# Kernel optimization log

Hardware: AMD Instinct MI355X
Metric: run time of the kernel (lower is better)

The kernel has to match this reference:

```python
import jax, jax.numpy as jnp
import numpy as np

N = 100000   # nodes
E = 1000000  # edges
F = 128      # num_features
H = 64       # hidden_size
C = 1        # num_classes
G = 128      # num graphs in batch


def gcn_conv(x, W, b, src, dst, deg_inv_sqrt):
    # PyG GCNConv: add self-loops, symmetric normalization D^-1/2 (A+I) D^-1/2, then X W + b
    h = x @ W                                   # [N, H]
    norm = deg_inv_sqrt[src] * deg_inv_sqrt[dst]  # [E]
    msg = h[src] * norm[:, None]                # gather + scale, [E, H]
    out = jnp.zeros_like(h).at[dst].add(msg)    # scatter-add to targets
    out = out + h * (deg_inv_sqrt ** 2)[:, None]  # self-loop contribution
    return out + b


def setup_inputs() -> dict:
    key = jax.random.key(0)
    ks = jax.random.split(key, 12)
    x = jax.random.normal(ks[0], (N, F), dtype=jnp.float32)
    edge_index = jax.random.randint(ks[1], (2, E), 0, N, dtype=jnp.int32).astype(jnp.int64)
    batch = jnp.sort(jax.random.randint(ks[2], (N,), 0, G, dtype=jnp.int32)).astype(jnp.int64)
    def glorot(k, fan_in, fan_out):
        s = np.float32(np.sqrt(6.0 / (fan_in + fan_out)))
        return jax.random.uniform(k, (fan_in, fan_out), jnp.float32, -s, s)
    return {
        "x": x, "edge_index": edge_index, "batch": batch,
        "W1": glorot(ks[3], F, H), "b1": jnp.zeros((H,), jnp.float32),
        "W2": glorot(ks[4], H, H), "b2": jnp.zeros((H,), jnp.float32),
        "Wl1": glorot(ks[5], H, H), "bl1": jnp.zeros((H,), jnp.float32),
        "Wl2": glorot(ks[6], H, C), "bl2": jnp.zeros((C,), jnp.float32),
    }


def reference(x, edge_index, batch, W1, b1, W2, b2, Wl1, bl1, Wl2, bl2):
    src, dst = edge_index[0], edge_index[1]
    # degree with self-loops: 1 + in-degree(target)
    deg = jnp.ones((N,), x.dtype).at[dst].add(jnp.ones((E,), x.dtype))
    deg_inv_sqrt = jax.lax.rsqrt(deg)
    h = jax.nn.relu(gcn_conv(x, W1, b1, src, dst, deg_inv_sqrt))
    h = jax.nn.relu(gcn_conv(h, W2, b2, src, dst, deg_inv_sqrt))
    g = jax.ops.segment_sum(h, batch, num_segments=G)  # global_add_pool, [G, H]
    g = jax.nn.relu(g @ Wl1 + bl1)
    out = g @ Wl2 + bl2                                # [G, 1]
    return out.squeeze(axis=1)                         # [G]
```

## Files before the change

### kernel.cpp

```cpp
#include <hip/hip_runtime.h>

#define NN 100000
#define EE 1000000
#define FF 128
#define HH 64
#define GG 128
#define NB 391

__device__ inline unsigned short f2bf(float f) {
    unsigned u = __float_as_uint(f);
    u += 0x7fffu + ((u >> 16) & 1u);
    return (unsigned short)(u >> 16);
}
__device__ inline float bf2f(unsigned short h) {
    return __uint_as_float((unsigned)h << 16);
}

__global__ void k_hist(const int* __restrict__ ei, int* __restrict__ cnt) {
    int e = blockIdx.x * 256 + threadIdx.x;
    if (e < EE) atomicAdd(&cnt[ei[EE + e]], 1);
}

__global__ void k_scan1(const int* __restrict__ cnt, int* __restrict__ part) {
    int i = blockIdx.x * 256 + threadIdx.x;
    int v = (i < NN) ? cnt[i] : 0;
    for (int o = 1; o < 64; o <<= 1) v += __shfl_xor(v, o);
    __shared__ int ws[4];
    if ((threadIdx.x & 63) == 0) ws[threadIdx.x >> 6] = v;
    __syncthreads();
    if (threadIdx.x == 0) part[blockIdx.x] = ws[0] + ws[1] + ws[2] + ws[3];
}

__global__ void k_scan2(int* __restrict__ part) {
    __shared__ int buf[512];
    int t = threadIdx.x;
    int v = (t < NB) ? part[t] : 0;
    buf[t] = v; __syncthreads();
    for (int o = 1; o < 512; o <<= 1) {
        int u = (t >= o) ? buf[t - o] : 0;
        __syncthreads();
        buf[t] += u;
        __syncthreads();
    }
    if (t < NB) part[t] = buf[t] - v;
}

__global__ void k_scan3(const int* __restrict__ cnt, const int* __restrict__ part,
                        int* __restrict__ row_ptr, int* __restrict__ cursor,
                        float* __restrict__ dis) {
    int i = blockIdx.x * 256 + threadIdx.x;
    int v = (i < NN) ? cnt[i] : 0;
    int lane = threadIdx.x & 63, w = threadIdx.x >> 6;
    int incl = v;
    for (int o = 1; o < 64; o <<= 1) { int u = __shfl_up(incl, o); if (lane >= o) incl += u; }
    __shared__ int ws[4];
    if (lane == 63) ws[w] = incl;
    __syncthreads();
    int woff = 0;
    for (int k = 0; k < w; ++k) woff += ws[k];
    int excl = incl - v + woff + part[blockIdx.x];
    if (i < NN) {
        row_ptr[i] = excl;
        cursor[i]  = excl;
        dis[i] = rsqrtf((float)(v + 1));
    }
    if (i == 0) row_ptr[NN] = EE;
}

__global__ void k_place(const int* __restrict__ ei, int* __restrict__ cursor,
                        int* __restrict__ srcs) {
    int e = blockIdx.x * 256 + threadIdx.x;
    if (e < EE) {
        int d = ei[EE + e];
        int p = atomicAdd(&cursor[d], 1);
        srcs[p] = ei[e];
    }
}

template<int K>
__global__ __launch_bounds__(256) void
k_matmul_b(const float* __restrict__ X, const float* __restrict__ W,
           const float* __restrict__ dis, unsigned short* __restrict__ Y) {
    __shared__ float Wl[K * HH];
    for (int i = threadIdx.x; i < K * HH; i += 256) Wl[i] = W[i];
    __syncthreads();
    const int lane = threadIdx.x & 63;
    const int wv   = threadIdx.x >> 6;
    const int c4   = (lane & 15) * 4;
    const int rsg  = lane >> 4;
    const int r0   = blockIdx.x * 64 + wv * 16 + rsg * 4;

    const float* xr0; const float* xr1; const float* xr2; const float* xr3;
    {
        int a = r0,     b_ = r0 + 1, c = r0 + 2, d = r0 + 3;
        if (a > NN - 1) a = NN - 1;
        if (b_ > NN - 1) b_ = NN - 1;
        if (c > NN - 1) c = NN - 1;
        if (d > NN - 1) d = NN - 1;
        xr0 = X + (size_t)a * K; xr1 = X + (size_t)b_ * K;
        xr2 = X + (size_t)c * K; xr3 = X + (size_t)d * K;
    }
    float4 acc0 = {0,0,0,0}, acc1 = {0,0,0,0}, acc2 = {0,0,0,0}, acc3 = {0,0,0,0};

#pragma unroll 8
    for (int k4 = 0; k4 < K / 4; ++k4) {
        const float4 x0 = *(const float4*)(xr0 + k4 * 4);
        const float4 x1 = *(const float4*)(xr1 + k4 * 4);
        const float4 x2 = *(const float4*)(xr2 + k4 * 4);
        const float4 x3 = *(const float4*)(xr3 + k4 * 4);
        const float4 w0 = *(const float4*)&Wl[(k4 * 4 + 0) * HH + c4];
        const float4 w1 = *(const float4*)&Wl[(k4 * 4 + 1) * HH + c4];
        const float4 w2 = *(const float4*)&Wl[(k4 * 4 + 2) * HH + c4];
        const float4 w3 = *(const float4*)&Wl[(k4 * 4 + 3) * HH + c4];
#define FMA4(A, XS) \
        A.x = fmaf(XS.x, w0.x, A.x); A.y = fmaf(XS.x, w0.y, A.y); \
        A.z = fmaf(XS.x, w0.z, A.z); A.w = fmaf(XS.x, w0.w, A.w); \
        A.x = fmaf(XS.y, w1.x, A.x); A.y = fmaf(XS.y, w1.y, A.y); \
        A.z = fmaf(XS.y, w1.z, A.z); A.w = fmaf(XS.y, w1.w, A.w); \
        A.x = fmaf(XS.z, w2.x, A.x); A.y = fmaf(XS.z, w2.y, A.y); \
        A.z = fmaf(XS.z, w2.z, A.z); A.w = fmaf(XS.z, w2.w, A.w); \
        A.x = fmaf(XS.w, w3.x, A.x); A.y = fmaf(XS.w, w3.y, A.y); \
        A.z = fmaf(XS.w, w3.z, A.z); A.w = fmaf(XS.w, w3.w, A.w);
        FMA4(acc0, x0) FMA4(acc1, x1) FMA4(acc2, x2) FMA4(acc3, x3)
#undef FMA4
    }
#define STORE(I, A) { \
        const int r = r0 + I; \
        if (r < NN) { \
            const float d = dis[r]; \
            ushort4 o; \
            o.x = f2bf(A.x * d); o.y = f2bf(A.y * d); \
            o.z = f2bf(A.z * d); o.w = f2bf(A.w * d); \
            *(ushort4*)(Y + (size_t)r * HH + c4) = o; \
        } }
    STORE(0, acc0) STORE(1, acc1) STORE(2, acc2) STORE(3, acc3)
#undef STORE
}

template<bool POOL>
__global__ __launch_bounds__(256) void
k_gconv(const int* __restrict__ row_ptr, const int* __restrict__ srcs,
        const float* __restrict__ dis, const unsigned short* __restrict__ Hs,
        const float* __restrict__ b, float* __restrict__ Out,
        const int* __restrict__ batch, float* __restrict__ g) {
    const int node = blockIdx.x * 4 + (threadIdx.x >> 6);
    const int lane = threadIdx.x & 63;
    const int li   = lane & 15;
    const int qr   = lane >> 4;
    const int p0   = row_ptr[node];
    const int deg  = row_ptr[node + 1] - p0;
    const int items  = deg + 1;
    const int nbatch = (items + 7) >> 3;

    float ac0 = 0.f, ac1 = 0.f, ac2 = 0.f, ac3 = 0.f;

#define IDX(bi, dA, dB) { \
        const int iA = 8 * (bi) + qr, iB = iA + 4; \
        dA = srcs[p0 + (iA < deg ? iA : 0)]; \
        dB = srcs[p0 + (iB < deg ? iB : 0)]; }
#define VAL(bi, sA, sB, vA, vB) { \
        const int iA = 8 * (bi) + qr, iB = iA + 4; \
        const int rA = (iA < deg) ? sA : node; \
        const int rB = (iB < deg) ? sB : node; \
        vA = *(const uint2*)(Hs + (size_t)rA * HH + li * 4); \
        vB = *(const uint2*)(Hs + (size_t)rB * HH + li * 4); }
#define CONSUME(bi, vA, vB) { \
        const int iA = 8 * (bi) + qr, iB = iA + 4; \
        const unsigned m0 = (iA <= deg) ? vA.x : 0u; \
        const unsigned m1 = (iA <= deg) ? vA.y : 0u; \
        const unsigned m2 = (iB <= deg) ? vB.x : 0u; \
        const unsigned m3 = (iB <= deg) ? vB.y : 0u; \
        ac0 += bf2f((unsigned short)m0);  ac1 += bf2f((unsigned short)(m0 >> 16)); \
        ac2 += bf2f((unsigned short)m1);  ac3 += bf2f((unsigned short)(m1 >> 16)); \
        ac0 += bf2f((unsigned short)m2);  ac1 += bf2f((unsigned short)(m2 >> 16)); \
        ac2 += bf2f((unsigned short)m3);  ac3 += bf2f((unsigned short)(m3 >> 16)); }

    int sA0, sA1, sB0, sB1;
    uint2 vA0, vA1;
    IDX(0, sA0, sA1);
    VAL(0, sA0, sA1, vA0, vA1);
    IDX(1, sB0, sB1);
    for (int bi = 1; bi < nbatch; ++bi) {
        uint2 vB0, vB1;
        VAL(bi, sB0, sB1, vB0, vB1);
        IDX(bi + 1, sB0, sB1);
        CONSUME(bi - 1, vA0, vA1);
        vA0 = vB0; vA1 = vB1;
    }
    CONSUME(nbatch - 1, vA0, vA1);
#undef IDX
#undef VAL
#undef CONSUME

    ac0 += __shfl_xor(ac0, 16); ac0 += __shfl_xor(ac0, 32);
    ac1 += __shfl_xor(ac1, 16); ac1 += __shfl_xor(ac1, 32);
    ac2 += __shfl_xor(ac2, 16); ac2 += __shfl_xor(ac2, 32);
    ac3 += __shfl_xor(ac3, 16); ac3 += __shfl_xor(ac3, 32);
    const float c0 = __shfl(ac0, lane >> 2);
    const float c1 = __shfl(ac1, lane >> 2);
    const float c2 = __shfl(ac2, lane >> 2);
    const float c3 = __shfl(ac3, lane >> 2);
    const int m = lane & 3;
    float acc = (m == 0) ? c0 : (m == 1) ? c1 : (m == 2) ? c2 : c3;

    const float dd = dis[node];
    float v = acc * dd + b[lane];
    v = fmaxf(v, 0.0f);
    if (POOL) {
        unsafeAtomicAdd(&g[(size_t)batch[node] * HH + lane], v);
    } else {
        Out[(size_t)node * HH + lane] = v;
    }
}

__global__ void k_head1(const float* __restrict__ g, const float* __restrict__ W,
                        const float* __restrict__ b, float* __restrict__ g2) {
    const int idx = blockIdx.x * 256 + threadIdx.x;
    const int row = idx >> 6;
    const int col = idx & 63;
    const float* gr = g + (size_t)row * HH;
    float acc = b[col];
#pragma unroll
    for (int k = 0; k < HH; ++k) acc = fmaf(gr[k], W[k * HH + col], acc);
    g2[idx] = acc > 0.0f ? acc : 0.0f;
}

__global__ void k_head2(const float* __restrict__ g2, const float* __restrict__ W,
                        const float* __restrict__ b, float* __restrict__ out) {
    const int r = threadIdx.x;
    if (r >= GG) return;
    const float* gr = g2 + (size_t)r * HH;
    float acc = 0.0f;
#pragma unroll
    for (int k = 0; k < HH; ++k) acc = fmaf(gr[k], W[k], acc);
    out[r] = acc + b[0];
}

extern "C" void kernel_launch(void* const* d_in, const int* in_sizes, int n_in,
                              void* d_out, int out_size, void* d_ws, size_t ws_size,
                              hipStream_t stream) {
    const float* x   = (const float*)d_in[0];
    const int*   ei  = (const int*)d_in[1];
    const int*   bat = (const int*)d_in[2];
    const float* W1  = (const float*)d_in[3];
    const float* b1  = (const float*)d_in[4];
    const float* W2  = (const float*)d_in[5];
    const float* b2  = (const float*)d_in[6];
    const float* Wl1 = (const float*)d_in[7];
    const float* bl1 = (const float*)d_in[8];
    const float* Wl2 = (const float*)d_in[9];
    const float* bl2 = (const float*)d_in[10];
    float* out = (float*)d_out;

    char* w = (char*)d_ws;
    float* dis     = (float*)(w);
    int*   cnt     = (int*)  (w + 400128);
    int*   row_ptr = (int*)  (w + 800256);
    int*   cursor  = (int*)  (w + 1200640);
    int*   part    = (int*)  (w + 1600768);
    int*   srcs    = (int*)  (w + 1602816);
    unsigned short* B = (unsigned short*)(w + 5602816);
    float* A       = (float*)(w + 31202816);
    float* g       = (float*)(w + 56802816);
    float* g2      = g + GG * HH;

    hipMemsetAsync(cnt, 0, (size_t)NN * sizeof(int), stream);
    k_hist <<<(EE + 255) / 256, 256, 0, stream>>>(ei, cnt);
    k_scan1<<<NB, 256, 0, stream>>>(cnt, part);
    k_scan2<<<1, 512, 0, stream>>>(part);
    k_scan3<<<NB, 256, 0, stream>>>(cnt, part, row_ptr, cursor, dis);
    k_place<<<(EE + 255) / 256, 256, 0, stream>>>(ei, cursor, srcs);

    k_matmul_b<FF><<<(NN + 63) / 64, 256, 0, stream>>>(x, W1, dis, B);
    k_gconv<false><<<NN / 4, 256, 0, stream>>>(row_ptr, srcs, dis, B, b1, A, nullptr, nullptr);

    k_matmul_b<HH><<<(NN + 63) / 64, 256, 0, stream>>>(A, W2, dis, B);
    hipMemsetAsync(g, 0, (size_t)GG * HH * sizeof(float), stream);
    k_gconv<true><<<NN / 4, 256, 0, stream>>>(row_ptr, srcs, dis, B, b2, nullptr, bat, g);

    k_head1<<<(GG * HH) / 256, 256, 0, stream>>>(g, Wl1, bl1, g2);
    k_head2<<<1, 128, 0, stream>>>(g2, Wl2, bl2, out);
}
```

Baseline: 319.6 us.

## Quantize hidden features to int8 with per-row scales and fuse edge placement into matmul

Stores the transformed node features as int8 with a per-row float scale instead of bf16, which halves the bytes gathered per edge in the graph-conv kernels. Merges the edge-placement kernel into the first matmul launch as extra blocks so the two run concurrently, and moves the degree rsqrt into the first scan kernel. The int8 quantization loses precision relative to bf16 and may push results past the tolerance. Because the MMB blocks launch before the placement blocks in one grid, the two kinds of work can overlap.

New measurement: 292.4 us. 8.5% less time.

```diff
diff --git a/kernel.cpp b/kernel.cpp
--- a/kernel.cpp
+++ b/kernel.cpp
@@ -6,24 +6,19 @@
 #define HH 64
 #define GG 128
 #define NB 391
-
-__device__ inline unsigned short f2bf(float f) {
-    unsigned u = __float_as_uint(f);
-    u += 0x7fffu + ((u >> 16) & 1u);
-    return (unsigned short)(u >> 16);
-}
-__device__ inline float bf2f(unsigned short h) {
-    return __uint_as_float((unsigned)h << 16);
-}
+#define MMB 1563
 
 __global__ void k_hist(const int* __restrict__ ei, int* __restrict__ cnt) {
     int e = blockIdx.x * 256 + threadIdx.x;
     if (e < EE) atomicAdd(&cnt[ei[EE + e]], 1);
 }
 
-__global__ void k_scan1(const int* __restrict__ cnt, int* __restrict__ part) {
+__global__ void k_scan1(const int* __restrict__ cnt, int* __restrict__ part,
+                        float* __restrict__ dis) {
     int i = blockIdx.x * 256 + threadIdx.x;
-    int v = (i < NN) ? cnt[i] : 0;
+    int c = (i < NN) ? cnt[i] : 0;
+    if (i < NN) dis[i] = rsqrtf((float)(c + 1));
+    int v = (i < NN) ? c : 0;
     for (int o = 1; o < 64; o <<= 1) v += __shfl_xor(v, o);
     __shared__ int ws[4];
     if ((threadIdx.x & 63) == 0) ws[threadIdx.x >> 6] = v;
@@ -46,8 +41,7 @@
 }
 
 __global__ void k_scan3(const int* __restrict__ cnt, const int* __restrict__ part,
-                        int* __restrict__ row_ptr, int* __restrict__ cursor,
-                        float* __restrict__ dis) {
+                        int* __restrict__ row_ptr, int* __restrict__ cursor) {
     int i = blockIdx.x * 256 + threadIdx.x;
     int v = (i < NN) ? cnt[i] : 0;
     int lane = threadIdx.x & 63, w = threadIdx.x >> 6;
@@ -62,33 +56,22 @@
     if (i < NN) {
         row_ptr[i] = excl;
         cursor[i]  = excl;
-        dis[i] = rsqrtf((float)(v + 1));
     }
     if (i == 0) row_ptr[NN] = EE;
 }
 
-__global__ void k_place(const int* __restrict__ ei, int* __restrict__ cursor,
-                        int* __restrict__ srcs) {
-    int e = blockIdx.x * 256 + threadIdx.x;
-    if (e < EE) {
-        int d = ei[EE + e];
-        int p = atomicAdd(&cursor[d], 1);
-        srcs[p] = ei[e];
-    }
-}
-
 template<int K>
-__global__ __launch_bounds__(256) void
-k_matmul_b(const float* __restrict__ X, const float* __restrict__ W,
-           const float* __restrict__ dis, unsigned short* __restrict__ Y) {
-    __shared__ float Wl[K * HH];
+__device__ __forceinline__ void
+mm_body(const float* __restrict__ X, const float* __restrict__ W,
+        const float* __restrict__ dis, unsigned* __restrict__ Y8,
+        float* __restrict__ S, float* __restrict__ Wl, int bid) {
     for (int i = threadIdx.x; i < K * HH; i += 256) Wl[i] = W[i];
     __syncthreads();
     const int lane = threadIdx.x & 63;
     const int wv   = threadIdx.x >> 6;
     const int c4   = (lane & 15) * 4;
     const int rsg  = lane >> 4;
-    const int r0   = blockIdx.x * 64 + wv * 16 + rsg * 4;
+    const int r0   = bid * 64 + wv * 16 + rsg * 4;
 
     const float* xr0; const float* xr1; const float* xr2; const float* xr3;
     {
@@ -128,21 +111,57 @@
         const int r = r0 + I; \
         if (r < NN) { \
             const float d = dis[r]; \
-            ushort4 o; \
-            o.x = f2bf(A.x * d); o.y = f2bf(A.y * d); \
-            o.z = f2bf(A.z * d); o.w = f2bf(A.w * d); \
-            *(ushort4*)(Y + (size_t)r * HH + c4) = o; \
+            const float ax = A.x * d, ay = A.y * d, az = A.z * d, aw = A.w * d; \
+            float m = fmaxf(fmaxf(fabsf(ax), fabsf(ay)), fmaxf(fabsf(az), fabsf(aw))); \
+            m = fmaxf(m, __shfl_xor(m, 1)); m = fmaxf(m, __shfl_xor(m, 2)); \
+            m = fmaxf(m, __shfl_xor(m, 4)); m = fmaxf(m, __shfl_xor(m, 8)); \
+            const float inv = 127.0f / m; \
+            int q0 = __float2int_rn(ax * inv), q1 = __float2int_rn(ay * inv); \
+            int q2 = __float2int_rn(az * inv), q3 = __float2int_rn(aw * inv); \
+            if (m == 0.0f) { q0 = q1 = q2 = q3 = 0; } \
+            const unsigned pk = (q0 & 0xff) | ((q1 & 0xff) << 8) | \
+                                ((q2 & 0xff) << 16) | ((q3 & 0xff) << 24); \
+            Y8[(size_t)r * 16 + (c4 >> 2)] = pk; \
+            if (c4 == 0) S[r] = m * (1.0f / 127.0f); \
         } }
     STORE(0, acc0) STORE(1, acc1) STORE(2, acc2) STORE(3, acc3)
 #undef STORE
 }
 
+template<int K>
+__global__ __launch_bounds__(256) void
+k_matmul_b(const float* __restrict__ X, const float* __restrict__ W,
+           const float* __restrict__ dis, unsigned* __restrict__ Y8,
+           float* __restrict__ S) {
+    __shared__ float Wl[K * HH];
+    mm_body<K>(X, W, dis, Y8, S, Wl, blockIdx.x);
+}
+
+__global__ __launch_bounds__(256) void
+k_mm1_place(const float* __restrict__ X, const float* __restrict__ W,
+            const float* __restrict__ dis, unsigned* __restrict__ Y8,
+            float* __restrict__ S, const int* __restrict__ ei,
+            int* __restrict__ cursor, int* __restrict__ srcs) {
+    __shared__ float Wl[FF * HH];
+    if (blockIdx.x < MMB) {
+        mm_body<FF>(X, W, dis, Y8, S, Wl, blockIdx.x);
+    } else {
+        int e = (blockIdx.x - MMB) * 256 + threadIdx.x;
+        if (e < EE) {
+            int d = ei[EE + e];
+            int p = atomicAdd(&cursor[d], 1);
+            srcs[p] = ei[e];
+        }
+    }
+}
+
 template<bool POOL>
 __global__ __launch_bounds__(256) void
 k_gconv(const int* __restrict__ row_ptr, const int* __restrict__ srcs,
-        const float* __restrict__ dis, const unsigned short* __restrict__ Hs,
-        const float* __restrict__ b, float* __restrict__ Out,
-        const int* __restrict__ batch, float* __restrict__ g) {
+        const float* __restrict__ dis, const unsigned* __restrict__ H8,
+        const float* __restrict__ S, const float* __restrict__ b,
+        float* __restrict__ Out, const int* __restrict__ batch,
+        float* __restrict__ g) {
     const int node = blockIdx.x * 4 + (threadIdx.x >> 6);
     const int lane = threadIdx.x & 63;
     const int li   = lane & 15;
@@ -158,36 +177,40 @@
         const int iA = 8 * (bi) + qr, iB = iA + 4; \
         dA = srcs[p0 + (iA < deg ? iA : 0)]; \
         dB = srcs[p0 + (iB < deg ? iB : 0)]; }
-#define VAL(bi, sA, sB, vA, vB) { \
+#define VAL(bi, sA, sB, vA, vB, gA, gB) { \
         const int iA = 8 * (bi) + qr, iB = iA + 4; \
         const int rA = (iA < deg) ? sA : node; \
         const int rB = (iB < deg) ? sB : node; \
-        vA = *(const uint2*)(Hs + (size_t)rA * HH + li * 4); \
-        vB = *(const uint2*)(Hs + (size_t)rB * HH + li * 4); }
-#define CONSUME(bi, vA, vB) { \
+        vA = H8[(size_t)rA * 16 + li];  gA = S[rA]; \
+        vB = H8[(size_t)rB * 16 + li];  gB = S[rB]; }
+#define CONSUME(bi, vA, vB, gA, gB) { \
         const int iA = 8 * (bi) + qr, iB = iA + 4; \
-        const unsigned m0 = (iA <= deg) ? vA.x : 0u; \
-        const unsigned m1 = (iA <= deg) ? vA.y : 0u; \
-        const unsigned m2 = (iB <= deg) ? vB.x : 0u; \
-        const unsigned m3 = (iB <= deg) ? vB.y : 0u; \
-        ac0 += bf2f((unsigned short)m0);  ac1 += bf2f((unsigned short)(m0 >> 16)); \
-        ac2 += bf2f((unsigned short)m1);  ac3 += bf2f((unsigned short)(m1 >> 16)); \
-        ac0 += bf2f((unsigned short)m2);  ac1 += bf2f((unsigned short)(m2 >> 16)); \
-        ac2 += bf2f((unsigned short)m3);  ac3 += bf2f((unsigned short)(m3 >> 16)); }
+        const float s0 = (iA <= deg) ? gA : 0.f; \
+        const float s1 = (iB <= deg) ? gB : 0.f; \
+        ac0 = fmaf(s0, (float)(signed char)(vA      ), ac0); \
+        ac1 = fmaf(s0, (float)(signed char)(vA >> 8 ), ac1); \
+        ac2 = fmaf(s0, (float)(signed char)(vA >> 16), ac2); \
+        ac3 = fmaf(s0, (float)(signed char)(vA >> 24), ac3); \
+        ac0 = fmaf(s1, (float)(signed char)(vB      ), ac0); \
+        ac1 = fmaf(s1, (float)(signed char)(vB >> 8 ), ac1); \
+        ac2 = fmaf(s1, (float)(signed char)(vB >> 16), ac2); \
+        ac3 = fmaf(s1, (float)(signed char)(vB >> 24), ac3); }
 
     int sA0, sA1, sB0, sB1;
-    uint2 vA0, vA1;
+    unsigned vA0, vA1;
+    float gA0, gA1;
     IDX(0, sA0, sA1);
-    VAL(0, sA0, sA1, vA0, vA1);
+    VAL(0, sA0, sA1, vA0, vA1, gA0, gA1);
     IDX(1, sB0, sB1);
     for (int bi = 1; bi < nbatch; ++bi) {
-        uint2 vB0, vB1;
-        VAL(bi, sB0, sB1, vB0, vB1);
+        unsigned vB0, vB1;
+        float gB0, gB1;
+        VAL(bi, sB0, sB1, vB0, vB1, gB0, gB1);
         IDX(bi + 1, sB0, sB1);
-        CONSUME(bi - 1, vA0, vA1);
-        vA0 = vB0; vA1 = vB1;
-    }
-    CONSUME(nbatch - 1, vA0, vA1);
+        CONSUME(bi - 1, vA0, vA1, gA0, gA1);
+        vA0 = vB0; vA1 = vB1; gA0 = gB0; gA1 = gB1;
+    }
+    CONSUME(nbatch - 1, vA0, vA1, gA0, gA1);
 #undef IDX
 #undef VAL
 #undef CONSUME
@@ -253,30 +276,30 @@
     float* out = (float*)d_out;
 
     char* w = (char*)d_ws;
-    float* dis     = (float*)(w);
-    int*   cnt     = (int*)  (w + 400128);
-    int*   row_ptr = (int*)  (w + 800256);
-    int*   cursor  = (int*)  (w + 1200640);
-    int*   part    = (int*)  (w + 1600768);
-    int*   srcs    = (int*)  (w + 1602816);
-    unsigned short* B = (unsigned short*)(w + 5602816);
-    float* A       = (float*)(w + 31202816);
-    float* g       = (float*)(w + 56802816);
-    float* g2      = g + GG * HH;
+    float*    dis     = (float*)(w);
+    int*      cnt     = (int*)  (w + 400128);
+    int*      row_ptr = (int*)  (w + 800256);
+    int*      cursor  = (int*)  (w + 1200640);
+    int*      part    = (int*)  (w + 1600768);
+    int*      srcs    = (int*)  (w + 1602816);
+    float*    S       = (float*)(w + 5602816);
+    unsigned* H8      = (unsigned*)(w + 6002944);
+    float*    A       = (float*)(w + 12402944);
+    float*    g       = (float*)(w + 38002944);
+    float*    g2      = g + GG * HH;
 
     hipMemsetAsync(cnt, 0, (size_t)NN * sizeof(int), stream);
     k_hist <<<(EE + 255) / 256, 256, 0, stream>>>(ei, cnt);
-    k_scan1<<<NB, 256, 0, stream>>>(cnt, part);
+    k_scan1<<<NB, 256, 0, stream>>>(cnt, part, dis);
     k_scan2<<<1, 512, 0, stream>>>(part);
-    k_scan3<<<NB, 256, 0, stream>>>(cnt, part, row_ptr, cursor, dis);
-    k_place<<<(EE + 255) / 256, 256, 0, stream>>>(ei, cursor, srcs);
-
-    k_matmul_b<FF><<<(NN + 63) / 64, 256, 0, stream>>>(x, W1, dis, B);
-    k_gconv<false><<<NN / 4, 256, 0, stream>>>(row_ptr, srcs, dis, B, b1, A, nullptr, nullptr);
-
-    k_matmul_b<HH><<<(NN + 63) / 64, 256, 0, stream>>>(A, W2, dis, B);
+    k_scan3<<<NB, 256, 0, stream>>>(cnt, part, row_ptr, cursor);
+
+    k_mm1_place<<<MMB + (EE + 255) / 256, 256, 0, stream>>>(x, W1, dis, H8, S, ei, cursor, srcs);
+    k_gconv<false><<<NN / 4, 256, 0, stream>>>(row_ptr, srcs, dis, H8, S, b1, A, nullptr, nullptr);
+
+    k_matmul_b<HH><<<(NN + 63) / 64, 256, 0, stream>>>(A, W2, dis, H8, S);
     hipMemsetAsync(g, 0, (size_t)GG * HH * sizeof(float), stream);
-    k_gconv<true><<<NN / 4, 256, 0, stream>>>(row_ptr, srcs, dis, B, b2, nullptr, bat, g);
+    k_gconv<true><<<NN / 4, 256, 0, stream>>>(row_ptr, srcs, dis, H8, S, b2, nullptr, bat, g);
 
     k_head1<<<(GG * HH) / 256, 256, 0, stream>>>(g, Wl1, bl1, g2);
     k_head2<<<1, 128, 0, stream>>>(g2, Wl2, bl2, out);
```
